# Performance work log

Measured on AMD Instinct MI355X. Metric: run time of the kernel, lower is better.

## Reference

```python
import jax, jax.numpy as jnp
import numpy as np

N_NODES = 100000
N_EDGES = 1000000
IN_DIM = 64
OUT_DIM = 64
EDGE_DIM = 16
LN_EPS = 1e-5
GINE_EPS = 0.0  # PyG GINEConv default eps


def setup_inputs() -> dict:
    key = jax.random.key(0)
    ks = jax.random.split(key, 10)
    s = lambda d: 1.0 / np.sqrt(d)
    x = jax.random.normal(ks[0], (N_NODES, IN_DIM), dtype=jnp.float32)
    edge_index = jax.random.randint(ks[1], (2, N_EDGES), 0, N_NODES, dtype=jnp.int64)
    edge_attr = jax.random.normal(ks[2], (N_EDGES, EDGE_DIM), dtype=jnp.float32)
    # GINEConv internal edge projection Linear(edge_dim, in_dim)
    We = jax.random.uniform(ks[3], (EDGE_DIM, IN_DIM), jnp.float32, -s(EDGE_DIM), s(EDGE_DIM))
    be = jax.random.uniform(ks[4], (IN_DIM,), jnp.float32, -s(EDGE_DIM), s(EDGE_DIM))
    # MLP: Linear(in_dim, out_dim) -> ReLU -> Linear(out_dim, out_dim)
    W1 = jax.random.uniform(ks[5], (IN_DIM, OUT_DIM), jnp.float32, -s(IN_DIM), s(IN_DIM))
    b1 = jax.random.uniform(ks[6], (OUT_DIM,), jnp.float32, -s(IN_DIM), s(IN_DIM))
    W2 = jax.random.uniform(ks[7], (OUT_DIM, OUT_DIM), jnp.float32, -s(OUT_DIM), s(OUT_DIM))
    b2 = jax.random.uniform(ks[8], (OUT_DIM,), jnp.float32, -s(OUT_DIM), s(OUT_DIM))
    ln_gamma = jnp.ones((OUT_DIM,), jnp.float32)
    ln_beta = jnp.zeros((OUT_DIM,), jnp.float32)
    return {"x": x, "edge_index": edge_index, "edge_attr": edge_attr,
            "We": We, "be": be, "W1": W1, "b1": b1, "W2": W2, "b2": b2,
            "ln_gamma": ln_gamma, "ln_beta": ln_beta}


def reference(x, edge_index, edge_attr, We, be, W1, b1, W2, b2, ln_gamma, ln_beta):
    src, dst = edge_index[0], edge_index[1]
    # message: ReLU(x_j + lin(edge_attr))  [E, IN_DIM]
    msg = jax.nn.relu(x[src] + edge_attr @ We + be)
    # scatter-sum into target nodes  [N, IN_DIM]
    aggr = jax.ops.segment_sum(msg, dst, num_segments=x.shape[0])
    h = (1.0 + GINE_EPS) * x + aggr
    # MLP
    h = jax.nn.relu(h @ W1 + b1) @ W2 + b2
    # LayerNorm over last dim
    mu = jnp.mean(h, axis=-1, keepdims=True)
    var = jnp.var(h, axis=-1, keepdims=True)
    h = (h - mu) * jax.lax.rsqrt(var + LN_EPS) * ln_gamma + ln_beta
    return jax.nn.relu(h)
```

## Files before the change

kernel.cpp:

```cpp
#include <hip/hip_runtime.h>

typedef short short8 __attribute__((ext_vector_type(8)));
typedef float f32x4 __attribute__((ext_vector_type(4)));

__device__ __forceinline__ float bf2f(unsigned short b) {
    union { unsigned u; float f; } c;
    c.u = ((unsigned)b) << 16;
    return c.f;
}

__device__ __forceinline__ unsigned short f2bf(float x) {
    union { float f; unsigned u; } c;
    c.f = x;
    unsigned u = c.u;
    u += 0x7fffu + ((u >> 16) & 1u);
    return (unsigned short)(u >> 16);
}

__device__ __forceinline__ float loadf(const void* p, long long i, unsigned isbf) {
    if (isbf) return bf2f(((const unsigned short*)p)[i]);
    return ((const float*)p)[i];
}

__device__ __forceinline__ f32x4 mfma16(short8 a, short8 b, f32x4 c) {
    return __builtin_amdgcn_mfma_f32_16x16x32_bf16(a, b, c, 0, 0, 0);
}

__device__ __forceinline__ float dotbf(uint4 ea, uint4 eb, const float* Wcol) {
    unsigned wds[8] = {ea.x, ea.y, ea.z, ea.w, eb.x, eb.y, eb.z, eb.w};
    float acc = 0.f;
    #pragma unroll
    for (int q = 0; q < 8; ++q) {
        union { unsigned u; float f; } clo, chi;
        clo.u = wds[q] << 16;
        chi.u = wds[q] & 0xffff0000u;
        acc += clo.f * Wcol[2 * q] + chi.f * Wcol[2 * q + 1];
    }
    return acc;
}

__device__ __forceinline__ float dotf32(const float* eap, const float* Wcol) {
    f32x4 e0 = ((const f32x4*)eap)[0];
    f32x4 e1 = ((const f32x4*)eap)[1];
    f32x4 e2 = ((const f32x4*)eap)[2];
    f32x4 e3 = ((const f32x4*)eap)[3];
    float ea[16] = {e0[0], e0[1], e0[2], e0[3],
                    e1[0], e1[1], e1[2], e1[3],
                    e2[0], e2[1], e2[2], e2[3],
                    e3[0], e3[1], e3[2], e3[3]};
    float acc = 0.f;
    #pragma unroll
    for (int k = 0; k < 16; ++k) acc += ea[k] * Wcol[k];
    return acc;
}

__global__ void gine_flag_kernel(const unsigned* gm_bits, const unsigned* ei_bits,
                                 unsigned* flags) {
    if (blockIdx.x == 0 && threadIdx.x == 0) {
        flags[0] = (gm_bits[0] == 0x3F803F80u) ? 1u : 0u;
        unsigned o = 0;
        for (int k = 0; k < 8; ++k) o |= ei_bits[2 * k + 1];
        flags[1] = (o == 0u) ? 1u : 0u;
    }
}

__global__ void gine_zero_kernel(float* p, int n) {
    int t = blockIdx.x * blockDim.x + threadIdx.x;
    if (t < n) p[t] = 0.0f;
}

__global__ void gine_prep_kernel(const void* W1, const void* b1,
                                 const void* W2, const void* b2,
                                 const void* gm, const void* bt,
                                 const void* We, const void* be,
                                 const unsigned* flags,
                                 unsigned short* W1B, unsigned short* W2B,
                                 float* vecs) {
    int t = blockIdx.x * blockDim.x + threadIdx.x;
    unsigned isbf = flags[0];
    if (t < 8192) {
        int which = t >> 12;
        int u = t & 4095;
        int j = u & 7, L = (u >> 3) & 63, ktnt = u >> 9;
        int kt = ktnt >> 2, nt = ktnt & 3;
        int k = kt * 32 + (L >> 4) * 8 + j;
        int c = nt * 16 + (L & 15);
        const void* W = which ? W2 : W1;
        unsigned short v = f2bf(loadf(W, k * 64 + c, isbf));
        if (which) W2B[u] = v; else W1B[u] = v;
    } else if (t < 8448) {
        int u = t - 8192;
        const void* s = (u < 64) ? b1 : (u < 128) ? b2 : (u < 192) ? gm : bt;
        vecs[u] = loadf(s, u & 63, isbf);
    } else if (t < 8512) {
        vecs[256 + (t - 8448)] = loadf(be, t - 8448, isbf);
    } else if (t < 9536) {
        int u = t - 8512;
        vecs[320 + u] = loadf(We, u, isbf);
    }
}

__global__ void gine_hinit_kernel(const void* x, float* h,
                                  const unsigned* flags, int total) {
    int t = blockIdx.x * blockDim.x + threadIdx.x;
    unsigned isbf = flags[0];
    if (isbf) {
        int i = t * 8;
        if (i >= total) return;
        uint4 v = *(const uint4*)((const unsigned short*)x + i);
        unsigned wds[4] = {v.x, v.y, v.z, v.w};
        #pragma unroll
        for (int q = 0; q < 4; ++q) {
            union { unsigned u; float f; } clo, chi;
            clo.u = wds[q] << 16;
            chi.u = wds[q] & 0xffff0000u;
            h[i + 2 * q]     = clo.f;
            h[i + 2 * q + 1] = chi.f;
        }
    } else {
        int i = t * 4;
        if (i >= total) return;
        f32x4 v = *(const f32x4*)((const float*)x + i);
        *(f32x4*)(h + i) = v;
    }
}

__global__ void gine_histS_kernel(const void* edge_index, const unsigned* flags,
                                  int* count, int E, int N) {
    int t = blockIdx.x * blockDim.x + threadIdx.x;
    int stride = gridDim.x * blockDim.x;
    unsigned is64 = flags[1];
    for (int e = t; e < E; e += stride) {
        long long src, dst;
        if (is64) {
            src = ((const long long*)edge_index)[e];
            dst = ((const long long*)edge_index)[E + e];
        } else {
            src = ((const int*)edge_index)[e];
            dst = ((const int*)edge_index)[E + e];
        }
        if (dst < 0 || dst >= N) continue;
        if (src < 0) src = 0;
        if (src >= N) src = N - 1;
        atomicAdd(&count[(int)src], 1);
    }
}

__global__ void gine_scan1_kernel(const int* count, int* row_start, int* bsum,
                                  int N) {
    __shared__ int s[256];
    int t = threadIdx.x;
    int i = blockIdx.x * 256 + t;
    int v = (i < N) ? count[i] : 0;
    s[t] = v;
    __syncthreads();
    for (int off = 1; off < 256; off <<= 1) {
        int u = (t >= off) ? s[t - off] : 0;
        __syncthreads();
        s[t] += u;
        __syncthreads();
    }
    if (i < N) row_start[i] = s[t] - v;
    if (t == 255) bsum[blockIdx.x] = s[255];
}

__global__ void gine_scan2_kernel(int* bsum, int* bscan, int* row_start,
                                  int nb, int N) {
    __shared__ int s[512];
    int t = threadIdx.x;
    int v = (t < nb) ? bsum[t] : 0;
    s[t] = v;
    __syncthreads();
    for (int off = 1; off < 512; off <<= 1) {
        int u = (t >= off) ? s[t - off] : 0;
        __syncthreads();
        s[t] += u;
        __syncthreads();
    }
    if (t < nb) bscan[t] = s[t] - v;
    if (t == nb - 1) row_start[N] = s[t];
}

__global__ void gine_scan3_kernel(int* row_start, int* cursor,
                                  const int* bscan, int N) {
    int i = blockIdx.x * 256 + threadIdx.x;
    if (i < N) {
        int r = row_start[i] + bscan[blockIdx.x];
        row_start[i] = r;
        cursor[i] = r;
    }
}

__global__ void gine_scatterS_kernel(const void* edge_index, const void* edge_attr,
                                     const unsigned* flags, int* cursor,
                                     unsigned long long* meta,
                                     unsigned short* eaS, int E, int N) {
    int t = blockIdx.x * blockDim.x + threadIdx.x;
    int stride = gridDim.x * blockDim.x;
    unsigned is64 = flags[1];
    unsigned isbf = flags[0];
    for (int e = t; e < E; e += stride) {
        long long src, dst;
        if (is64) {
            src = ((const long long*)edge_index)[e];
            dst = ((const long long*)edge_index)[E + e];
        } else {
            src = ((const int*)edge_index)[e];
            dst = ((const int*)edge_index)[E + e];
        }
        if (dst < 0 || dst >= N) continue;
        if (src < 0) src = 0;
        if (src >= N) src = N - 1;
        int pos = atomicAdd(&cursor[(int)src], 1);
        meta[pos] = ((unsigned long long)(unsigned)e << 32)
                  | (unsigned long long)(unsigned)dst;
        if (isbf) {
            const uint4* er = (const uint4*)((const unsigned short*)edge_attr
                                             + (size_t)e * 16);
            uint4 r0 = er[0];
            uint4 r1 = er[1];
            uint4* wp = (uint4*)(eaS + (size_t)pos * 16);
            wp[0] = r0;
            wp[1] = r1;
        }
    }
}

__global__ __launch_bounds__(256) void gine_spray_kernel(
        const void* x, const void* edge_attr,
        const unsigned long long* meta, const unsigned short* eaS,
        const int* rowS, const float* vecs, const unsigned* flags,
        float* h, int N) {
    int w = threadIdx.x >> 6;
    int lane = threadIdx.x & 63;
    int gw = blockIdx.x * 4 + w;
    int nwaves = gridDim.x * 4;
    unsigned isbf = flags[0];

    float Wcol[16];
    #pragma unroll
    for (int k = 0; k < 16; ++k) Wcol[k] = vecs[320 + k * 64 + lane];
    float bev = vecs[256 + lane];

    if (isbf) {
        const unsigned short* xb = (const unsigned short*)x;
        for (int s = gw; s < N; s += nwaves) {
            int beg = rowS[s];
            int end = rowS[s + 1];
            if (beg == end) continue;
            float xv = bf2f(xb[(size_t)s * 64 + lane]) + bev;
            int j = beg;
            for (; j + 2 <= end; j += 2) {
                unsigned long long m0m = meta[j];
                unsigned long long m1m = meta[j + 1];
                int dst0 = (int)(m0m & 0xffffffffULL);
                int dst1 = (int)(m1m & 0xffffffffULL);
                const uint4* p = (const uint4*)(eaS + (size_t)j * 16);
                uint4 e00 = p[0], e01 = p[1];
                uint4 e10 = p[2], e11 = p[3];
                float m0 = dotbf(e00, e01, Wcol) + xv;
                float m1 = dotbf(e10, e11, Wcol) + xv;
                if (m0 < 0.f) m0 = 0.f;
                if (m1 < 0.f) m1 = 0.f;
                atomicAdd(&h[(size_t)dst0 * 64 + lane], m0);
                atomicAdd(&h[(size_t)dst1 * 64 + lane], m1);
            }
            if (j < end) {
                unsigned long long mm = meta[j];
                int dst = (int)(mm & 0xffffffffULL);
                const uint4* p = (const uint4*)(eaS + (size_t)j * 16);
                uint4 e0 = p[0], e1 = p[1];
                float m = dotbf(e0, e1, Wcol) + xv;
                if (m < 0.f) m = 0.f;
                atomicAdd(&h[(size_t)dst * 64 + lane], m);
            }
        }
    } else {
        const float* xf  = (const float*)x;
        const float* eaf = (const float*)edge_attr;
        for (int s = gw; s < N; s += nwaves) {
            int beg = rowS[s];
            int end = rowS[s + 1];
            if (beg == end) continue;
            float xv = xf[(size_t)s * 64 + lane] + bev;
            for (int j = beg; j < end; ++j) {
                unsigned long long mm = meta[j];
                int dst = (int)(mm & 0xffffffffULL);
                int eid = (int)(mm >> 32);
                float m = dotf32(eaf + (size_t)eid * 16, Wcol) + xv;
                if (m < 0.f) m = 0.f;
                atomicAdd(&h[(size_t)dst * 64 + lane], m);
            }
        }
    }
}

__global__ void gine_hist_kernel(const void* edge_index, const unsigned* flags,
                                 int* count, int E, int N) {
    int t = blockIdx.x * blockDim.x + threadIdx.x;
    int stride = gridDim.x * blockDim.x;
    unsigned is64 = flags[1];
    for (int e = t; e < E; e += stride) {
        long long dst = is64 ? ((const long long*)edge_index)[E + e]
                             : (long long)((const int*)edge_index)[E + e];
        if (dst >= 0 && dst < N) atomicAdd(&count[(int)dst], 1);
    }
}

__global__ void gine_scatter_kernel(const void* edge_index, const unsigned* flags,
                                    int* cursor, unsigned long long* sorted,
                                    int E, int N) {
    int t = blockIdx.x * blockDim.x + threadIdx.x;
    int stride = gridDim.x * blockDim.x;
    unsigned is64 = flags[1];
    for (int e = t; e < E; e += stride) {
        long long src, dst;
        if (is64) {
            src = ((const long long*)edge_index)[e];
            dst = ((const long long*)edge_index)[E + e];
        } else {
            src = ((const int*)edge_index)[e];
            dst = ((const int*)edge_index)[E + e];
        }
        if (dst < 0 || dst >= N) continue;
        if (src < 0) src = 0;
        if (src >= N) src = N - 1;
        int pos = atomicAdd(&cursor[(int)dst], 1);
        sorted[pos] = ((unsigned long long)(unsigned)e << 32) | (unsigned long long)(unsigned)src;
    }
}

__global__ __launch_bounds__(256, 4) void gine_gather_kernel(
        const void* x, const void* edge_attr,
        const unsigned long long* sorted,
        const int* row_start, const float* vecs,
        const unsigned* flags, float* h, int N) {
    int w = threadIdx.x >> 6;
    int lane = threadIdx.x & 63;
    int gw = blockIdx.x * 4 + w;
    int nwaves = gridDim.x * 4;
    unsigned isbf = flags[0];

    float Wcol[16];
    #pragma unroll
    for (int k = 0; k < 16; ++k) Wcol[k] = vecs[320 + k * 64 + lane];
    float bev = vecs[256 + lane];

    if (isbf) {
        const unsigned short* xb  = (const unsigned short*)x;
        const unsigned short* eab = (const unsigned short*)edge_attr;
        for (int v = gw; v < N; v += nwaves) {
            int beg = row_start[v];
            int end = row_start[v + 1];
            float a0 = bf2f(xb[(size_t)v * 64 + lane]);
            float a1 = 0.f, a2 = 0.f, a3 = 0.f;
            int i = beg;
            for (; i + 4 <= end; i += 4) {
                unsigned long long c0 = sorted[i];
                unsigned long long c1 = sorted[i + 1];
                unsigned long long c2 = sorted[i + 2];
                unsigned long long c3 = sorted[i + 3];
                int src0 = (int)(c0 & 0xffffffffULL), eid0 = (int)(c0 >> 32);
                int src1 = (int)(c1 & 0xffffffffULL), eid1 = (int)(c1 >> 32);
                int src2 = (int)(c2 & 0xffffffffULL), eid2 = (int)(c2 >> 32);
                int src3 = (int)(c3 & 0xffffffffULL), eid3 = (int)(c3 >> 32);

                float xv0 = bf2f(xb[(size_t)src0 * 64 + lane]);
                float xv1 = bf2f(xb[(size_t)src1 * 64 + lane]);
                float xv2 = bf2f(xb[(size_t)src2 * 64 + lane]);
                float xv3 = bf2f(xb[(size_t)src3 * 64 + lane]);

                const uint4* p0 = (const uint4*)(eab + (size_t)eid0 * 16);
                const uint4* p1 = (const uint4*)(eab + (size_t)eid1 * 16);
                const uint4* p2 = (const uint4*)(eab + (size_t)eid2 * 16);
                const uint4* p3 = (const uint4*)(eab + (size_t)eid3 * 16);
                uint4 e00 = p0[0], e01 = p0[1];
                uint4 e10 = p1[0], e11 = p1[1];
                uint4 e20 = p2[0], e21 = p2[1];
                uint4 e30 = p3[0], e31 = p3[1];

                float m0 = dotbf(e00, e01, Wcol);
                float m1 = dotbf(e10, e11, Wcol);
                float m2 = dotbf(e20, e21, Wcol);
                float m3 = dotbf(e30, e31, Wcol);
                m0 += bev + xv0; if (m0 < 0.f) m0 = 0.f; a0 += m0;
                m1 += bev + xv1; if (m1 < 0.f) m1 = 0.f; a1 += m1;
                m2 += bev + xv2; if (m2 < 0.f) m2 = 0.f; a2 += m2;
                m3 += bev + xv3; if (m3 < 0.f) m3 = 0.f; a3 += m3;
            }
            for (; i < end; ++i) {
                unsigned long long c = sorted[i];
                int src = (int)(c & 0xffffffffULL);
                int eid = (int)(c >> 32);
                float xv = bf2f(xb[(size_t)src * 64 + lane]);
                const uint4* p0 = (const uint4*)(eab + (size_t)eid * 16);
                uint4 e0 = p0[0], e1 = p0[1];
                float m = dotbf(e0, e1, Wcol);
                m += bev + xv;
                if (m < 0.f) m = 0.f;
                a0 += m;
            }
            h[(long long)v * 64 + lane] = (a0 + a1) + (a2 + a3);
        }
    } else {
        const float* xf  = (const float*)x;
        const float* eaf = (const float*)edge_attr;
        for (int v = gw; v < N; v += nwaves) {
            int beg = row_start[v];
            int end = row_start[v + 1];
            float a0 = xf[(size_t)v * 64 + lane];
            float a1 = 0.f;
            int i = beg;
            for (; i + 2 <= end; i += 2) {
                unsigned long long c0 = sorted[i];
                unsigned long long c1 = sorted[i + 1];
                int src0 = (int)(c0 & 0xffffffffULL), eid0 = (int)(c0 >> 32);
                int src1 = (int)(c1 & 0xffffffffULL), eid1 = (int)(c1 >> 32);
                float xv0 = xf[(size_t)src0 * 64 + lane];
                float xv1 = xf[(size_t)src1 * 64 + lane];
                float m0 = dotf32(eaf + (size_t)eid0 * 16, Wcol);
                float m1 = dotf32(eaf + (size_t)eid1 * 16, Wcol);
                m0 += bev + xv0; if (m0 < 0.f) m0 = 0.f; a0 += m0;
                m1 += bev + xv1; if (m1 < 0.f) m1 = 0.f; a1 += m1;
            }
            for (; i < end; ++i) {
                unsigned long long c = sorted[i];
                int src = (int)(c & 0xffffffffULL);
                int eid = (int)(c >> 32);
                float xv = xf[(size_t)src * 64 + lane];
                float m = dotf32(eaf + (size_t)eid * 16, Wcol);
                m += bev + xv;
                if (m < 0.f) m = 0.f;
                a0 += m;
            }
            h[(long long)v * 64 + lane] = a0 + a1;
        }
    }
}

__global__ void GINEBlock_49795850830259_kernel(
    const void* x, const void* edge_index, const void* edge_attr,
    const void* We, const void* be, const unsigned* flags,
    float* aggr, int E, int N, int n0, int n1) {
    int wid  = (blockIdx.x * blockDim.x + threadIdx.x) >> 6;
    int lane = threadIdx.x & 63;
    if (wid >= E) return;

    unsigned isbf = flags[0];
    unsigned is64 = flags[1];

    long long src, dst;
    if (is64) {
        src = ((const long long*)edge_index)[wid];
        dst = ((const long long*)edge_index)[E + wid];
    } else {
        src = ((const int*)edge_index)[wid];
        dst = ((const int*)edge_index)[E + wid];
    }
    if (src < 0 || src >= N || dst < n0 || dst >= n1) return;

    float eav = 0.0f;
    if (lane < 16) eav = loadf(edge_attr, (long long)wid * 16 + lane, isbf);

    float acc = loadf(be, lane, isbf);
    for (int k = 0; k < 16; ++k)
        acc += __shfl(eav, k, 64) * loadf(We, k * 64 + lane, isbf);

    acc += loadf(x, src * 64 + lane, isbf);
    if (acc < 0.0f) acc = 0.0f;

    atomicAdd(aggr + (dst - n0) * 64 + lane, acc);
}

__global__ void gine_addx_kernel(const void* x, float* aggr,
                                 const unsigned* flags, int n0, int n1) {
    int t = blockIdx.x * blockDim.x + threadIdx.x;
    int total = (n1 - n0) * 64;
    if (t >= total) return;
    unsigned isbf = flags[0];
    aggr[t] += loadf(x, (long long)n0 * 64 + t, isbf);
}

__global__ __launch_bounds__(256) void gine_node_mfma_kernel(
    const float* h, const unsigned short* W1B, const unsigned short* W2B,
    const float* vecs, const unsigned* flags, void* out, int n0, int n1) {
    __shared__ float Tlds[4][16 * 68];
    int w = threadIdx.x >> 6;
    int L = threadIdx.x & 63;
    int g = L >> 4, m = L & 15;
    int nb = n0 + (blockIdx.x * 4 + w) * 16;
    if (nb >= n1) return;
    unsigned isbf = flags[0];

    const float* b1f = vecs;
    const float* b2f = vecs + 64;
    const float* gmf = vecs + 128;
    const float* btf = vecs + 192;

    int node = nb + m;
    if (node >= n1) node = n1 - 1;
    long long rel = node - n0;

    short8 ahi[2], alo[2];
    for (int kt = 0; kt < 2; ++kt) {
        int fb = kt * 32 + g * 8;
        const float* hp = h + rel * 64 + fb;
        f32x4 a0 = *(const f32x4*)hp;
        f32x4 a1 = *(const f32x4*)(hp + 4);
        for (int j = 0; j < 8; ++j) {
            float hv = (j < 4) ? a0[j] : a1[j - 4];
            unsigned short hb = f2bf(hv);
            float lo = hv - bf2f(hb);
            ahi[kt][j] = (short)hb;
            alo[kt][j] = (short)f2bf(lo);
        }
    }

    float t16[16];
    for (int nt = 0; nt < 4; ++nt) {
        short8 bp0 = *(const short8*)(W1B + ((size_t)(0 * 4 + nt) * 64 + L) * 8);
        short8 bp1 = *(const short8*)(W1B + ((size_t)(1 * 4 + nt) * 64 + L) * 8);
        f32x4 acc = {0.f, 0.f, 0.f, 0.f};
        acc = mfma16(ahi[0], bp0, acc);
        acc = mfma16(ahi[1], bp1, acc);
        acc = mfma16(alo[0], bp0, acc);
        acc = mfma16(alo[1], bp1, acc);
        float bias = b1f[nt * 16 + m];
        for (int r = 0; r < 4; ++r) {
            float v = acc[r] + bias;
            t16[nt * 4 + r] = v > 0.f ? v : 0.f;
        }
    }

    float* tl = Tlds[w];
    for (int nt = 0; nt < 4; ++nt)
        for (int r = 0; r < 4; ++r)
            tl[(g * 4 + r) * 68 + nt * 16 + m] = t16[nt * 4 + r];

    short8 thi[2], tlo[2];
    for (int kt = 0; kt < 2; ++kt) {
        const float* rp = tl + m * 68 + kt * 32 + g * 8;
        f32x4 v0 = *(const f32x4*)rp;
        f32x4 v1 = *(const f32x4*)(rp + 4);
        for (int j = 0; j < 8; ++j) {
            float hv = (j < 4) ? v0[j] : v1[j - 4];
            unsigned short hb = f2bf(hv);
            float lo = hv - bf2f(hb);
            thi[kt][j] = (short)hb;
            tlo[kt][j] = (short)f2bf(lo);
        }
    }

    float o16[16];
    for (int nt = 0; nt < 4; ++nt) {
        short8 bp0 = *(const short8*)(W2B + ((size_t)(0 * 4 + nt) * 64 + L) * 8);
        short8 bp1 = *(const short8*)(W2B + ((size_t)(1 * 4 + nt) * 64 + L) * 8);
        f32x4 acc = {0.f, 0.f, 0.f, 0.f};
        acc = mfma16(thi[0], bp0, acc);
        acc = mfma16(thi[1], bp1, acc);
        acc = mfma16(tlo[0], bp0, acc);
        acc = mfma16(tlo[1], bp1, acc);
        float bias = b2f[nt * 16 + m];
        for (int r = 0; r < 4; ++r) o16[nt * 4 + r] = acc[r] + bias;
    }

    for (int r = 0; r < 4; ++r) {
        float s = o16[r] + o16[4 + r] + o16[8 + r] + o16[12 + r];
        s += __shfl_xor(s, 1, 64);
        s += __shfl_xor(s, 2, 64);
        s += __shfl_xor(s, 4, 64);
        s += __shfl_xor(s, 8, 64);
        float mu = s * (1.0f / 64.0f);
        float v = 0.f;
        for (int nt = 0; nt < 4; ++nt) {
            float d = o16[nt * 4 + r] - mu;
            v += d * d;
        }
        v += __shfl_xor(v, 1, 64);
        v += __shfl_xor(v, 2, 64);
        v += __shfl_xor(v, 4, 64);
        v += __shfl_xor(v, 8, 64);
        float inv = rsqrtf(v * (1.0f / 64.0f) + 1e-5f);
        int nodeR = nb + g * 4 + r;
        if (nodeR < n1) {
            for (int nt = 0; nt < 4; ++nt) {
                int c = nt * 16 + m;
                float rr = (o16[nt * 4 + r] - mu) * inv * gmf[c] + btf[c];
                if (rr < 0.f) rr = 0.f;
                long long oidx = (long long)nodeR * 64 + c;
                if (isbf) ((unsigned short*)out)[oidx] = f2bf(rr);
                else      ((float*)out)[oidx] = rr;
            }
        }
    }
}

static inline size_t align256(size_t a) { return (a + 255) & ~(size_t)255; }

extern "C" void kernel_launch(void* const* d_in, const int* in_sizes, int n_in,
                              void* d_out, int out_size, void* d_ws, size_t ws_size,
                              hipStream_t stream) {
    const void* x          = d_in[0];
    const void* edge_index = d_in[1];
    const void* edge_attr  = d_in[2];
    const void* We         = d_in[3];
    const void* be         = d_in[4];
    const void* W1         = d_in[5];
    const void* b1         = d_in[6];
    const void* W2         = d_in[7];
    const void* b2         = d_in[8];
    const void* gm         = d_in[9];
    const void* bt         = d_in[10];

    const int N = in_sizes[0] / 64;
    const int E = in_sizes[1] / 2;

    unsigned* flags     = (unsigned*)d_ws;
    unsigned short* W1B = (unsigned short*)((char*)d_ws + 256);
    unsigned short* W2B = W1B + 4096;
    float* vecs         = (float*)(W2B + 4096);
    int* bsum           = (int*)((char*)d_ws + 24576);
    int* bscan          = bsum + 1024;

    gine_flag_kernel<<<1, 64, 0, stream>>>((const unsigned*)gm,
                                           (const unsigned*)edge_index, flags);
    gine_prep_kernel<<<38, 256, 0, stream>>>(W1, b1, W2, b2, gm, bt, We, be,
                                             flags, W1B, W2B, vecs);

    int nb = (N + 255) / 256;
    int node_blocks = (N + 63) / 64;
    int gblocks = (N + 15) / 16;
    if (gblocks > 6250) gblocks = 6250;
    int total = N * 64;

    size_t o_count  = 32768;
    size_t o_row    = o_count + align256((size_t)N * 4);
    size_t o_cursor = o_row + align256((size_t)(N + 1) * 4);
    size_t o_meta   = o_cursor + align256((size_t)N * 4);
    size_t o_eas    = o_meta + align256((size_t)E * 8);
    size_t o_hA     = o_eas + align256((size_t)E * 32);
    size_t o_hB     = o_eas;
    size_t needA    = o_hA + (size_t)N * 256;
    size_t needB    = o_hB + (size_t)N * 256;

    if (ws_size >= needA && nb <= 512) {
        int* count     = (int*)((char*)d_ws + o_count);
        int* rowS      = (int*)((char*)d_ws + o_row);
        int* cursorS   = (int*)((char*)d_ws + o_cursor);
        unsigned long long* meta = (unsigned long long*)((char*)d_ws + o_meta);
        unsigned short* eaS      = (unsigned short*)((char*)d_ws + o_eas);
        float* h       = (float*)((char*)d_ws + o_hA);

        gine_zero_kernel<<<(N + 255) / 256, 256, 0, stream>>>((float*)count, N);
        gine_hinit_kernel<<<(total / 4 + 255) / 256, 256, 0, stream>>>(
            x, h, flags, total);
        gine_histS_kernel<<<1024, 256, 0, stream>>>(edge_index, flags, count, E, N);
        gine_scan1_kernel<<<nb, 256, 0, stream>>>(count, rowS, bsum, N);
        gine_scan2_kernel<<<1, 512, 0, stream>>>(bsum, bscan, rowS, nb, N);
        gine_scan3_kernel<<<nb, 256, 0, stream>>>(rowS, cursorS, bscan, N);
        gine_scatterS_kernel<<<1024, 256, 0, stream>>>(edge_index, edge_attr,
                                                       flags, cursorS, meta,
                                                       eaS, E, N);
        gine_spray_kernel<<<gblocks, 256, 0, stream>>>(x, edge_attr, meta, eaS,
                                                       rowS, vecs, flags, h, N);
        gine_node_mfma_kernel<<<node_blocks, 256, 0, stream>>>(
            h, W1B, W2B, vecs, flags, d_out, 0, N);
        return;
    }

    if (ws_size >= needB && nb <= 512) {
        int* count    = (int*)((char*)d_ws + o_count);
        int* row_start= (int*)((char*)d_ws + o_row);
        int* cursor   = (int*)((char*)d_ws + o_cursor);
        unsigned long long* sorted = (unsigned long long*)((char*)d_ws + o_meta);
        float* h      = (float*)((char*)d_ws + o_hB);

        gine_zero_kernel<<<(N + 255) / 256, 256, 0, stream>>>((float*)count, N);
        gine_hist_kernel<<<1024, 256, 0, stream>>>(edge_index, flags, count, E, N);
        gine_scan1_kernel<<<nb, 256, 0, stream>>>(count, row_start, bsum, N);
        gine_scan2_kernel<<<1, 512, 0, stream>>>(bsum, bscan, row_start, nb, N);
        gine_scan3_kernel<<<nb, 256, 0, stream>>>(row_start, cursor, bscan, N);
        gine_scatter_kernel<<<1024, 256, 0, stream>>>(edge_index, flags, cursor,
                                                      sorted, E, N);
        gine_gather_kernel<<<gblocks, 256, 0, stream>>>(x, edge_attr, sorted,
                                                        row_start, vecs, flags,
                                                        h, N);
        gine_node_mfma_kernel<<<node_blocks, 256, 0, stream>>>(
            h, W1B, W2B, vecs, flags, d_out, 0, N);
        return;
    }

    float* aggr = (float*)((char*)d_ws + 32768);
    long long usable = (ws_size > 32768) ? (long long)(ws_size - 32768) : 0;
    long long ncll = (usable / 256) & ~63LL;
    int NC = (ncll > N) ? N : (int)ncll;
    if (NC < 64) return;

    long long edge_threads = (long long)E * 64;
    int edge_blocks = (int)((edge_threads + 255) / 256);

    for (int n0 = 0; n0 < N; n0 += NC) {
        int n1 = n0 + NC; if (n1 > N) n1 = N;
        int chunk = n1 - n0;
        int n_aggr = chunk * 64;

        gine_zero_kernel<<<(n_aggr + 255) / 256, 256, 0, stream>>>(aggr, n_aggr);
        GINEBlock_49795850830259_kernel<<<edge_blocks, 256, 0, stream>>>(
            x, edge_index, edge_attr, We, be, flags, aggr, E, N, n0, n1);
        gine_addx_kernel<<<(n_aggr + 255) / 256, 256, 0, stream>>>(
            x, aggr, flags, n0, n1);
        int chunk_blocks = (chunk + 63) / 64;
        gine_node_mfma_kernel<<<chunk_blocks, 256, 0, stream>>>(
            aggr, W1B, W2B, vecs, flags, d_out, n0, n1);
    }
}
```

Before: 530.9 us.

## Split edges into dst-sorted gather half and src-sorted spray half

Partitions the edges into two halves. The first half is bucketed by destination and gathered with per-node register accumulation and a single atomic per node. The second half keeps the source-sorted spray with per-edge atomics. The hybrid kernel interleaves the two roles across alternating blocks so atomic-heavy and gather-heavy work run side by side. The cost is a second histogram and scan chain, two extra scatter buffers, and random x reads for the gathered half.

```diff
diff --git a/kernel.cpp b/kernel.cpp
--- a/kernel.cpp
+++ b/kernel.cpp
@@ -125,8 +125,8 @@
     }
 }
 
-__global__ void gine_histS_kernel(const void* edge_index, const unsigned* flags,
-                                  int* count, int E, int N) {
+__global__ void gine_hist2_kernel(const void* edge_index, const unsigned* flags,
+                                  int* countD, int* countS, int E, int Eh, int N) {
     int t = blockIdx.x * blockDim.x + threadIdx.x;
     int stride = gridDim.x * blockDim.x;
     unsigned is64 = flags[1];
@@ -142,7 +142,8 @@
         if (dst < 0 || dst >= N) continue;
         if (src < 0) src = 0;
         if (src >= N) src = N - 1;
-        atomicAdd(&count[(int)src], 1);
+        if (e < Eh) atomicAdd(&countD[(int)dst], 1);
+        else        atomicAdd(&countS[(int)src], 1);
     }
 }
 
@@ -191,10 +192,14 @@
     }
 }
 
-__global__ void gine_scatterS_kernel(const void* edge_index, const void* edge_attr,
-                                     const unsigned* flags, int* cursor,
-                                     unsigned long long* meta,
-                                     unsigned short* eaS, int E, int N) {
+__global__ void gine_scatter3_kernel(const void* edge_index, const void* edge_attr,
+                                     const unsigned* flags,
+                                     int* curD, int* curS,
+                                     unsigned long long* sortedD,
+                                     unsigned short* eaD,
+                                     unsigned long long* metaS,
+                                     unsigned short* eaS,
+                                     int E, int Eh, int N) {
     int t = blockIdx.x * blockDim.x + threadIdx.x;
     int stride = gridDim.x * blockDim.x;
     unsigned is64 = flags[1];
@@ -211,30 +216,50 @@
         if (dst < 0 || dst >= N) continue;
         if (src < 0) src = 0;
         if (src >= N) src = N - 1;
-        int pos = atomicAdd(&cursor[(int)src], 1);
-        meta[pos] = ((unsigned long long)(unsigned)e << 32)
-                  | (unsigned long long)(unsigned)dst;
+
+        uint4 r0, r1;
         if (isbf) {
             const uint4* er = (const uint4*)((const unsigned short*)edge_attr
                                              + (size_t)e * 16);
-            uint4 r0 = er[0];
-            uint4 r1 = er[1];
-            uint4* wp = (uint4*)(eaS + (size_t)pos * 16);
-            wp[0] = r0;
-            wp[1] = r1;
-        }
-    }
-}
-
-__global__ __launch_bounds__(256) void gine_spray_kernel(
+            r0 = er[0];
+            r1 = er[1];
+        }
+        if (e < Eh) {
+            int pos = atomicAdd(&curD[(int)dst], 1);
+            sortedD[pos] = ((unsigned long long)(unsigned)e << 32)
+                         | (unsigned long long)(unsigned)src;
+            if (isbf) {
+                uint4* wp = (uint4*)(eaD + (size_t)pos * 16);
+                wp[0] = r0;
+                wp[1] = r1;
+            }
+        } else {
+            int pos = atomicAdd(&curS[(int)src], 1);
+            metaS[pos] = ((unsigned long long)(unsigned)e << 32)
+                       | (unsigned long long)(unsigned)dst;
+            if (isbf) {
+                uint4* wp = (uint4*)(eaS + (size_t)pos * 16);
+                wp[0] = r0;
+                wp[1] = r1;
+            }
+        }
+    }
+}
+
+__global__ __launch_bounds__(256) void gine_hybrid_kernel(
         const void* x, const void* edge_attr,
-        const unsigned long long* meta, const unsigned short* eaS,
-        const int* rowS, const float* vecs, const unsigned* flags,
-        float* h, int N) {
+        const unsigned long long* sortedD, const unsigned short* eaD,
+        const int* rowD,
+        const unsigned long long* metaS, const unsigned short* eaS,
+        const int* rowS,
+        const float* vecs, const unsigned* flags, float* h, int N) {
     int w = threadIdx.x >> 6;
     int lane = threadIdx.x & 63;
-    int gw = blockIdx.x * 4 + w;
-    int nwaves = gridDim.x * 4;
+    int role = blockIdx.x & 1;
+    int rb   = blockIdx.x >> 1;
+    int nrb  = gridDim.x >> 1;
+    int gw = rb * 4 + w;
+    int nwaves = nrb * 4;
     unsigned isbf = flags[0];
 
     float Wcol[16];
@@ -242,54 +267,114 @@
     for (int k = 0; k < 16; ++k) Wcol[k] = vecs[320 + k * 64 + lane];
     float bev = vecs[256 + lane];
 
-    if (isbf) {
-        const unsigned short* xb = (const unsigned short*)x;
-        for (int s = gw; s < N; s += nwaves) {
-            int beg = rowS[s];
-            int end = rowS[s + 1];
-            if (beg == end) continue;
-            float xv = bf2f(xb[(size_t)s * 64 + lane]) + bev;
-            int j = beg;
-            for (; j + 2 <= end; j += 2) {
-                unsigned long long m0m = meta[j];
-                unsigned long long m1m = meta[j + 1];
-                int dst0 = (int)(m0m & 0xffffffffULL);
-                int dst1 = (int)(m1m & 0xffffffffULL);
-                const uint4* p = (const uint4*)(eaS + (size_t)j * 16);
-                uint4 e00 = p[0], e01 = p[1];
-                uint4 e10 = p[2], e11 = p[3];
-                float m0 = dotbf(e00, e01, Wcol) + xv;
-                float m1 = dotbf(e10, e11, Wcol) + xv;
-                if (m0 < 0.f) m0 = 0.f;
-                if (m1 < 0.f) m1 = 0.f;
-                atomicAdd(&h[(size_t)dst0 * 64 + lane], m0);
-                atomicAdd(&h[(size_t)dst1 * 64 + lane], m1);
-            }
-            if (j < end) {
-                unsigned long long mm = meta[j];
-                int dst = (int)(mm & 0xffffffffULL);
-                const uint4* p = (const uint4*)(eaS + (size_t)j * 16);
-                uint4 e0 = p[0], e1 = p[1];
-                float m = dotbf(e0, e1, Wcol) + xv;
-                if (m < 0.f) m = 0.f;
-                atomicAdd(&h[(size_t)dst * 64 + lane], m);
+    if (role == 0) {
+        if (isbf) {
+            const unsigned short* xb = (const unsigned short*)x;
+            for (int v = gw; v < N; v += nwaves) {
+                int beg = rowD[v];
+                int end = rowD[v + 1];
+                if (beg == end) continue;
+                float a0 = 0.f, a1 = 0.f;
+                int i = beg;
+                for (; i + 2 <= end; i += 2) {
+                    unsigned long long c0 = sortedD[i];
+                    unsigned long long c1 = sortedD[i + 1];
+                    int src0 = (int)(c0 & 0xffffffffULL);
+                    int src1 = (int)(c1 & 0xffffffffULL);
+                    const uint4* p = (const uint4*)(eaD + (size_t)i * 16);
+                    uint4 e00 = p[0], e01 = p[1];
+                    uint4 e10 = p[2], e11 = p[3];
+                    float xv0 = bf2f(xb[(size_t)src0 * 64 + lane]);
+                    float xv1 = bf2f(xb[(size_t)src1 * 64 + lane]);
+                    float m0 = dotbf(e00, e01, Wcol) + bev + xv0;
+                    float m1 = dotbf(e10, e11, Wcol) + bev + xv1;
+                    if (m0 < 0.f) m0 = 0.f;
+                    if (m1 < 0.f) m1 = 0.f;
+                    a0 += m0;
+                    a1 += m1;
+                }
+                if (i < end) {
+                    unsigned long long c = sortedD[i];
+                    int src = (int)(c & 0xffffffffULL);
+                    const uint4* p = (const uint4*)(eaD + (size_t)i * 16);
+                    uint4 e0 = p[0], e1 = p[1];
+                    float xv = bf2f(xb[(size_t)src * 64 + lane]);
+                    float m = dotbf(e0, e1, Wcol) + bev + xv;
+                    if (m < 0.f) m = 0.f;
+                    a0 += m;
+                }
+                atomicAdd(&h[(size_t)v * 64 + lane], a0 + a1);
+            }
+        } else {
+            const float* xf  = (const float*)x;
+            const float* eaf = (const float*)edge_attr;
+            for (int v = gw; v < N; v += nwaves) {
+                int beg = rowD[v];
+                int end = rowD[v + 1];
+                if (beg == end) continue;
+                float a0 = 0.f;
+                for (int i = beg; i < end; ++i) {
+                    unsigned long long c = sortedD[i];
+                    int src = (int)(c & 0xffffffffULL);
+                    int eid = (int)(c >> 32);
+                    float xv = xf[(size_t)src * 64 + lane];
+                    float m = dotf32(eaf + (size_t)eid * 16, Wcol) + bev + xv;
+                    if (m < 0.f) m = 0.f;
+                    a0 += m;
+                }
+                atomicAdd(&h[(size_t)v * 64 + lane], a0);
             }
         }
     } else {
-        const float* xf  = (const float*)x;
-        const float* eaf = (const float*)edge_attr;
-        for (int s = gw; s < N; s += nwaves) {
-            int beg = rowS[s];
-            int end = rowS[s + 1];
-            if (beg == end) continue;
-            float xv = xf[(size_t)s * 64 + lane] + bev;
-            for (int j = beg; j < end; ++j) {
-                unsigned long long mm = meta[j];
-                int dst = (int)(mm & 0xffffffffULL);
-                int eid = (int)(mm >> 32);
-                float m = dotf32(eaf + (size_t)eid * 16, Wcol) + xv;
-                if (m < 0.f) m = 0.f;
-                atomicAdd(&h[(size_t)dst * 64 + lane], m);
+        if (isbf) {
+            const unsigned short* xb = (const unsigned short*)x;
+            for (int s = gw; s < N; s += nwaves) {
+                int beg = rowS[s];
+                int end = rowS[s + 1];
+                if (beg == end) continue;
+                float xv = bf2f(xb[(size_t)s * 64 + lane]) + bev;
+                int j = beg;
+                for (; j + 2 <= end; j += 2) {
+                    unsigned long long m0m = metaS[j];
+                    unsigned long long m1m = metaS[j + 1];
+                    int dst0 = (int)(m0m & 0xffffffffULL);
+                    int dst1 = (int)(m1m & 0xffffffffULL);
+                    const uint4* p = (const uint4*)(eaS + (size_t)j * 16);
+                    uint4 e00 = p[0], e01 = p[1];
+                    uint4 e10 = p[2], e11 = p[3];
+                    float m0 = dotbf(e00, e01, Wcol) + xv;
+                    float m1 = dotbf(e10, e11, Wcol) + xv;
+                    if (m0 < 0.f) m0 = 0.f;
+                    if (m1 < 0.f) m1 = 0.f;
+                    atomicAdd(&h[(size_t)dst0 * 64 + lane], m0);
+                    atomicAdd(&h[(size_t)dst1 * 64 + lane], m1);
+                }
+                if (j < end) {
+                    unsigned long long mm = metaS[j];
+                    int dst = (int)(mm & 0xffffffffULL);
+                    const uint4* p = (const uint4*)(eaS + (size_t)j * 16);
+                    uint4 e0 = p[0], e1 = p[1];
+                    float m = dotbf(e0, e1, Wcol) + xv;
+                    if (m < 0.f) m = 0.f;
+                    atomicAdd(&h[(size_t)dst * 64 + lane], m);
+                }
+            }
+        } else {
+            const float* xf  = (const float*)x;
+            const float* eaf = (const float*)edge_attr;
+            for (int s = gw; s < N; s += nwaves) {
+                int beg = rowS[s];
+                int end = rowS[s + 1];
+                if (beg == end) continue;
+                float xv = xf[(size_t)s * 64 + lane] + bev;
+                for (int j = beg; j < end; ++j) {
+                    unsigned long long mm = metaS[j];
+                    int dst = (int)(mm & 0xffffffffULL);
+                    int eid = (int)(mm >> 32);
+                    float m = dotf32(eaf + (size_t)eid * 16, Wcol) + xv;
+                    if (m < 0.f) m = 0.f;
+                    atomicAdd(&h[(size_t)dst * 64 + lane], m);
+                }
             }
         }
     }
@@ -614,6 +699,7 @@
 
     const int N = in_sizes[0] / 64;
     const int E = in_sizes[1] / 2;
+    const int Eh = E / 2;
 
     unsigned* flags     = (unsigned*)d_ws;
     unsigned short* W1B = (unsigned short*)((char*)d_ws + 256);
@@ -633,47 +719,68 @@
     if (gblocks > 6250) gblocks = 6250;
     int total = N * 64;
 
+    size_t a_countD = 32768;
+    size_t a_countS = a_countD + align256((size_t)N * 4);
+    size_t a_rowD   = a_countS + align256((size_t)N * 4);
+    size_t a_rowS   = a_rowD + align256((size_t)(N + 1) * 4);
+    size_t a_sortD  = a_rowS + align256((size_t)(N + 1) * 4);
+    size_t a_metaS  = a_sortD + align256((size_t)Eh * 8);
+    size_t a_eaD    = a_metaS + align256((size_t)(E - Eh) * 8);
+    size_t a_eaS    = a_eaD + align256((size_t)Eh * 32);
+    size_t a_h      = a_eaS + align256((size_t)(E - Eh) * 32);
+    size_t needA2   = a_h + (size_t)N * 256;
+
+    if (ws_size >= needA2 && nb <= 512) {
+        int* countD = (int*)((char*)d_ws + a_countD);
+        int* countS = (int*)((char*)d_ws + a_countS);
+        int* rowD   = (int*)((char*)d_ws + a_rowD);
+        int* rowS   = (int*)((char*)d_ws + a_rowS);
+        int* curD   = countD;
+        int* curS   = countS;
+        unsigned long long* sortedD = (unsigned long long*)((char*)d_ws + a_sortD);
+        unsigned long long* metaS   = (unsigned long long*)((char*)d_ws + a_metaS);
+        unsigned short* eaD = (unsigned short*)((char*)d_ws + a_eaD);
+        unsigned short* eaS = (unsigned short*)((char*)d_ws + a_eaS);
+        float* h    = (float*)((char*)d_ws + a_h);
+
+        gine_zero_kernel<<<(N + 255) / 256, 256, 0, stream>>>((float*)countD, N);
+        gine_zero_kernel<<<(N + 255) / 256, 256, 0, stream>>>((float*)countS, N);
+        gine_hinit_kernel<<<(total / 4 + 255) / 256, 256, 0, stream>>>(
+            x, h, flags, total);
+        gine_hist2_kernel<<<1024, 256, 0, stream>>>(edge_index, flags, countD,
+                                                    countS, E, Eh, N);
+        gine_scan1_kernel<<<nb, 256, 0, stream>>>(countD, rowD, bsum, N);
+        gine_scan2_kernel<<<1, 512, 0, stream>>>(bsum, bscan, rowD, nb, N);
+        gine_scan3_kernel<<<nb, 256, 0, stream>>>(rowD, curD, bscan, N);
+        gine_scan1_kernel<<<nb, 256, 0, stream>>>(countS, rowS, bsum, N);
+        gine_scan2_kernel<<<1, 512, 0, stream>>>(bsum, bscan, rowS, nb, N);
+        gine_scan3_kernel<<<nb, 256, 0, stream>>>(rowS, curS, bscan, N);
+        gine_scatter3_kernel<<<1024, 256, 0, stream>>>(edge_index, edge_attr,
+                                                       flags, curD, curS,
+                                                       sortedD, eaD, metaS, eaS,
+                                                       E, Eh, N);
+        gine_hybrid_kernel<<<6144, 256, 0, stream>>>(x, edge_attr,
+                                                     sortedD, eaD, rowD,
+                                                     metaS, eaS, rowS,
+                                                     vecs, flags, h, N);
+        gine_node_mfma_kernel<<<node_blocks, 256, 0, stream>>>(
+            h, W1B, W2B, vecs, flags, d_out, 0, N);
+        return;
+    }
+
     size_t o_count  = 32768;
     size_t o_row    = o_count + align256((size_t)N * 4);
     size_t o_cursor = o_row + align256((size_t)(N + 1) * 4);
-    size_t o_meta   = o_cursor + align256((size_t)N * 4);
-    size_t o_eas    = o_meta + align256((size_t)E * 8);
-    size_t o_hA     = o_eas + align256((size_t)E * 32);
-    size_t o_hB     = o_eas;
-    size_t needA    = o_hA + (size_t)N * 256;
-    size_t needB    = o_hB + (size_t)N * 256;
-
-    if (ws_size >= needA && nb <= 512) {
-        int* count     = (int*)((char*)d_ws + o_count);
-        int* rowS      = (int*)((char*)d_ws + o_row);
-        int* cursorS   = (int*)((char*)d_ws + o_cursor);
-        unsigned long long* meta = (unsigned long long*)((char*)d_ws + o_meta);
-        unsigned short* eaS      = (unsigned short*)((char*)d_ws + o_eas);
-        float* h       = (float*)((char*)d_ws + o_hA);
-
-        gine_zero_kernel<<<(N + 255) / 256, 256, 0, stream>>>((float*)count, N);
-        gine_hinit_kernel<<<(total / 4 + 255) / 256, 256, 0, stream>>>(
-            x, h, flags, total);
-        gine_histS_kernel<<<1024, 256, 0, stream>>>(edge_index, flags, count, E, N);
-        gine_scan1_kernel<<<nb, 256, 0, stream>>>(count, rowS, bsum, N);
-        gine_scan2_kernel<<<1, 512, 0, stream>>>(bsum, bscan, rowS, nb, N);
-        gine_scan3_kernel<<<nb, 256, 0, stream>>>(rowS, cursorS, bscan, N);
-        gine_scatterS_kernel<<<1024, 256, 0, stream>>>(edge_index, edge_attr,
-                                                       flags, cursorS, meta,
-                                                       eaS, E, N);
-        gine_spray_kernel<<<gblocks, 256, 0, stream>>>(x, edge_attr, meta, eaS,
-                                                       rowS, vecs, flags, h, N);
-        gine_node_mfma_kernel<<<node_blocks, 256, 0, stream>>>(
-            h, W1B, W2B, vecs, flags, d_out, 0, N);
-        return;
-    }
+    size_t o_sorted = o_cursor + align256((size_t)N * 4);
+    size_t o_h      = o_sorted + align256((size_t)E * 8);
+    size_t needB    = o_h + (size_t)N * 256;
 
     if (ws_size >= needB && nb <= 512) {
         int* count    = (int*)((char*)d_ws + o_count);
         int* row_start= (int*)((char*)d_ws + o_row);
         int* cursor   = (int*)((char*)d_ws + o_cursor);
-        unsigned long long* sorted = (unsigned long long*)((char*)d_ws + o_meta);
-        float* h      = (float*)((char*)d_ws + o_hB);
+        unsigned long long* sorted = (unsigned long long*)((char*)d_ws + o_sorted);
+        float* h      = (float*)((char*)d_ws + o_h);
 
         gine_zero_kernel<<<(N + 255) / 256, 256, 0, stream>>>((float*)count, N);
         gine_hist_kernel<<<1024, 256, 0, stream>>>(edge_index, flags, count, E, N);
```

Measured after the change: 595.2 us. +12.1%, slower.
